# Performance work log

Measured on AMD Instinct MI355X. Metric: run time of the kernel, lower is better.

Reference implementation:

```python
import jax, jax.numpy as jnp
import numpy as np

EPS = 1e-13

def masked_softmax(scores, mask):
    # scores: [B, L1, L2], mask: [B, L2] binary float
    # ESIM-style: softmax(scores * mask) * mask, renormalized.
    m = mask[:, None, :]                      # [B, 1, L2]
    r = jax.nn.softmax(scores * m, axis=-1) * m
    return r / (r.sum(axis=-1, keepdims=True) + EPS)

def weighted_sum(attn, tensor, mask):
    # attn: [B, L1, L2], tensor: [B, L2, D], mask: [B, L1]
    return jnp.matmul(attn, tensor) * mask[:, :, None]

def setup_inputs() -> dict:
    key = jax.random.key(0)
    k1, k2, k3, k4 = jax.random.split(key, 4)
    B, Lp, Lh, D = 64, 512, 512, 600
    encoded_premise = jax.random.normal(k1, (B, Lp, D), dtype=jnp.float32)
    encoded_hypothesis = jax.random.normal(k2, (B, Lh, D), dtype=jnp.float32)
    # binary padding masks (1 = valid token)
    premise_mask = (jax.random.uniform(k3, (B, Lp)) > 0.15).astype(jnp.float32)
    hypothesis_mask = (jax.random.uniform(k4, (B, Lh)) > 0.15).astype(jnp.float32)
    return {"encoded_premise": encoded_premise, "premise_mask": premise_mask,
            "encoded_hypothesis": encoded_hypothesis, "hypothesis_mask": hypothesis_mask}

def reference(encoded_premise, premise_mask, encoded_hypothesis, hypothesis_mask):
    # shared cross-attention score matrix [B, Lp, Lh]
    attn = jnp.einsum('bpd,bhd->bph', encoded_premise, encoded_hypothesis)
    a_p = masked_softmax(attn, hypothesis_mask)                    # [B, Lp, Lh]
    a_h = masked_softmax(attn.transpose(0, 2, 1), premise_mask)    # [B, Lh, Lp]
    weighted_premise = weighted_sum(a_p, encoded_hypothesis, premise_mask)      # [B, Lp, D]
    weighted_hypothesis = weighted_sum(a_h, encoded_premise, hypothesis_mask)   # [B, Lh, D]
    return (weighted_premise, weighted_hypothesis)
```

## Files before the change

### kernel.cpp

```cpp
#include <hip/hip_runtime.h>
#include <hip/hip_bf16.h>

#define DEVB 64
#define LSEQ 512
#define DDIM 600

typedef short short8 __attribute__((ext_vector_type(8)));
typedef float f32x4 __attribute__((ext_vector_type(4)));
typedef _Float16 f16x8 __attribute__((ext_vector_type(8)));
typedef _Float16 f16x4 __attribute__((ext_vector_type(4)));

constexpr int LDP = 40;

__device__ __forceinline__ unsigned short f2bf(float x) {
    union { float f; unsigned u; } v; v.f = x;
    unsigned r = v.u + 0x7fffu + ((v.u >> 16) & 1u);
    return (unsigned short)(r >> 16);
}
__device__ __forceinline__ f32x4 mfma16(short8 a, short8 b, f32x4 c) {
    return __builtin_amdgcn_mfma_f32_16x16x32_bf16(a, b, c, 0, 0, 0);
}
__device__ __forceinline__ f32x4 mfma16h(f16x8 a, f16x8 b, f32x4 c) {
    return __builtin_amdgcn_mfma_f32_16x16x32_f16(a, b, c, 0, 0, 0);
}

__global__ __launch_bounds__(256) void prep_t(
    const float* __restrict__ X, _Float16* __restrict__ Xhi,
    _Float16* __restrict__ Xlo, _Float16* __restrict__ XT)
{
    int blk = blockIdx.x;
    int b   = blk / 80;
    int rem = blk % 80;
    int r0  = (rem / 10) << 6;
    int d0  = (rem % 10) << 6;
    const float* Xb = X + (size_t)b * LSEQ * DDIM;
    _Float16* Hib = Xhi + (size_t)b * LSEQ * DDIM;
    _Float16* Lob = Xlo ? (Xlo + (size_t)b * LSEQ * DDIM) : nullptr;

    __shared__ _Float16 T[64 * 66];
    int t = threadIdx.x;
#pragma unroll
    for (int it = 0; it < 4; ++it) {
        int g  = t + (it << 8);
        int ri = g >> 4;
        int dc = (g & 15) << 2;
        if (d0 + dc < DDIM) {
            float4 x = *(const float4*)(Xb + (size_t)(r0 + ri) * DDIM + d0 + dc);
            f16x4 hi, lo;
            hi[0] = (_Float16)x.x; lo[0] = (_Float16)(x.x - (float)hi[0]);
            hi[1] = (_Float16)x.y; lo[1] = (_Float16)(x.y - (float)hi[1]);
            hi[2] = (_Float16)x.z; lo[2] = (_Float16)(x.z - (float)hi[2]);
            hi[3] = (_Float16)x.w; lo[3] = (_Float16)(x.w - (float)hi[3]);
            *(f16x4*)(Hib + (size_t)(r0 + ri) * DDIM + d0 + dc) = hi;
            if (Lob) *(f16x4*)(Lob + (size_t)(r0 + ri) * DDIM + d0 + dc) = lo;
            T[(dc + 0) * 66 + ri] = hi[0];
            T[(dc + 1) * 66 + ri] = hi[1];
            T[(dc + 2) * 66 + ri] = hi[2];
            T[(dc + 3) * 66 + ri] = hi[3];
        }
    }
    if (XT) {
        __syncthreads();
        int d  = t >> 2;
        int ch = (t & 3) << 4;
        if (d0 + d < DDIM) {
            unsigned buf[8];
#pragma unroll
            for (int i = 0; i < 8; ++i)
                buf[i] = *(const unsigned*)&T[d * 66 + ch + 2 * i];
            unsigned* dst = (unsigned*)(XT + ((size_t)b * DDIM + d0 + d) * LSEQ + r0 + ch);
            *(uint4*)(dst)     = *(uint4*)&buf[0];
            *(uint4*)(dst + 4) = *(uint4*)&buf[4];
        }
    }
}

__global__ __launch_bounds__(256) void attn_gemm(
    const _Float16* __restrict__ Phi, const _Float16* __restrict__ Plo,
    const _Float16* __restrict__ Hhi, float* __restrict__ attn)
{
    const int bid = blockIdx.x;
    const int swz = (bid & 7) * 128 + (bid >> 3);
    const int b  = swz >> 4;
    const int pt = ((swz >> 2) & 3) << 7;
    const int ht = (swz & 3) << 7;
    const _Float16* Pbh = Phi + ((size_t)b * LSEQ + pt) * DDIM;
    const _Float16* Pbl = Plo + ((size_t)b * LSEQ + pt) * DDIM;
    const _Float16* Hb  = Hhi + ((size_t)b * LSEQ + ht) * DDIM;
    float* Ab = attn + (size_t)b * LSEQ * LSEQ;

    __shared__ _Float16 Ah[2][128 * LDP], Al[2][128 * LDP], Bh[2][128 * LDP];

    const int t    = threadIdx.x;
    const int lane = t & 63;
    const int wave = t >> 6;
    const int wm = (wave >> 1) << 6;
    const int wn = (wave & 1) << 6;
    const int fr = lane & 15;
    const int fq = lane >> 4;
    const int srow = t >> 2;
    const int sc8  = (t & 3) << 3;

    f16x8 pf[6];
    const f16x8 zz = {0, 0, 0, 0, 0, 0, 0, 0};
    auto issue = [&](int k0) {
        bool ok = (k0 + sc8) < DDIM;
#pragma unroll
        for (int r = 0; r < 2; ++r) {
            size_t off = (size_t)(srow + (r << 6)) * DDIM + k0 + sc8;
            pf[r * 3 + 0] = ok ? *(const f16x8*)(Pbh + off) : zz;
            pf[r * 3 + 1] = ok ? *(const f16x8*)(Pbl + off) : zz;
            pf[r * 3 + 2] = ok ? *(const f16x8*)(Hb  + off) : zz;
        }
    };
    auto wr = [&](int buf) {
#pragma unroll
        for (int r = 0; r < 2; ++r) {
            int row = srow + (r << 6);
            *(f16x8*)&Ah[buf][row * LDP + sc8] = pf[r * 3 + 0];
            *(f16x8*)&Al[buf][row * LDP + sc8] = pf[r * 3 + 1];
            *(f16x8*)&Bh[buf][row * LDP + sc8] = pf[r * 3 + 2];
        }
    };

    issue(0);
    wr(0);
    issue(32);
    __syncthreads();

    f32x4 acc[4][4];
#pragma unroll
    for (int i = 0; i < 4; ++i)
#pragma unroll
        for (int j = 0; j < 4; ++j) acc[i][j] = (f32x4){0.f, 0.f, 0.f, 0.f};

    constexpr int NK = 19;
    int cur = 0;
    for (int it = 0; it < NK; ++it) {
        f16x8 ah[4], al[4], bh[4];
#pragma unroll
        for (int i = 0; i < 4; ++i) {
            ah[i] = *(const f16x8*)&Ah[cur][(wm + (i << 4) + fr) * LDP + (fq << 3)];
            al[i] = *(const f16x8*)&Al[cur][(wm + (i << 4) + fr) * LDP + (fq << 3)];
            bh[i] = *(const f16x8*)&Bh[cur][(wn + (i << 4) + fr) * LDP + (fq << 3)];
        }
        if (it + 1 < NK) {
            wr(cur ^ 1);
            if (it + 2 < NK) issue((it + 2) << 5);
        }
#pragma unroll
        for (int mi = 0; mi < 4; ++mi)
#pragma unroll
            for (int ni = 0; ni < 4; ++ni) {
                f32x4 c = acc[mi][ni];
                c = mfma16h(ah[mi], bh[ni], c);
                c = mfma16h(al[mi], bh[ni], c);
                acc[mi][ni] = c;
            }
        __syncthreads();
        cur ^= 1;
    }

#pragma unroll
    for (int mi = 0; mi < 4; ++mi)
#pragma unroll
        for (int ni = 0; ni < 4; ++ni)
#pragma unroll
            for (int j = 0; j < 4; ++j) {
                int p = pt + wm + (mi << 4) + (fq << 2) + j;
                int h = ht + wn + (ni << 4) + fr;
                Ab[(size_t)p * LSEQ + h] = acc[mi][ni][j];
            }
}

__global__ __launch_bounds__(256) void stats_w1(
    const float* __restrict__ attn, const float* __restrict__ hmask,
    const float* __restrict__ pmask,
    float* __restrict__ M1, float* __restrict__ R1,
    _Float16* __restrict__ W1,
    float* __restrict__ Mp, float* __restrict__ Tp, float* __restrict__ Sp)
{
    int b      = blockIdx.x >> 3;
    int stripe = blockIdx.x & 7;
    int lane   = threadIdx.x & 63;
    int wave   = threadIdx.x >> 6;
    const float* hm = hmask + (b << 9);
    const float* pm = pmask + (b << 9);

    float4 m0 = *(const float4*)(hm + (lane << 3));
    float4 m1 = *(const float4*)(hm + (lane << 3) + 4);
    float mk[8] = {m0.x, m0.y, m0.z, m0.w, m1.x, m1.y, m1.z, m1.w};

    float cM[8], cT[8], cS[8];
#pragma unroll
    for (int j = 0; j < 8; ++j) { cM[j] = -1e30f; cT[j] = 0.f; cS[j] = 0.f; }

    for (int i = 0; i < 16; ++i) {
        int row   = (stripe << 6) + (wave << 4) + i;
        int rowid = (b << 9) + row;
        const float* rp = attn + (size_t)rowid * LSEQ + (lane << 3);
        float4 s0 = *(const float4*)rp;
        float4 s1 = *(const float4*)(rp + 4);
        float s[8] = {s0.x, s0.y, s0.z, s0.w, s1.x, s1.y, s1.z, s1.w};

        float v[8];
#pragma unroll
        for (int j = 0; j < 8; ++j) v[j] = s[j] * mk[j];
        float mx = -1e30f;
#pragma unroll
        for (int j = 0; j < 8; ++j) mx = fmaxf(mx, v[j]);
#pragma unroll
        for (int off = 32; off; off >>= 1) mx = fmaxf(mx, __shfl_xor(mx, off));

        float e[8], T = 0.f, S = 0.f;
#pragma unroll
        for (int j = 0; j < 8; ++j) { e[j] = __expf(v[j] - mx); T += mk[j] * e[j]; S += e[j]; }
#pragma unroll
        for (int off = 32; off; off >>= 1) { T += __shfl_xor(T, off); S += __shfl_xor(S, off); }
        float R = 1.f / (T + 1e-13f * S);

        if (W1) {
            union { f16x8 v8; _Float16 h[8]; } wv;
#pragma unroll
            for (int j = 0; j < 8; ++j) wv.h[j] = (_Float16)(mk[j] * e[j] * R);
            *(f16x8*)(W1 + (size_t)rowid * LSEQ + (lane << 3)) = wv.v8;
        }
        if (lane == 0) { M1[rowid] = mx; R1[rowid] = R; }

        float pmv = pm[row];
#pragma unroll
        for (int j = 0; j < 8; ++j) {
            float v2 = s[j] * pmv;
            float nm = fmaxf(cM[j], v2);
            float sc = __expf(cM[j] - nm);
            float e2 = __expf(v2 - nm);
            cT[j] = cT[j] * sc + pmv * e2;
            cS[j] = cS[j] * sc + e2;
            cM[j] = nm;
        }
    }

    __shared__ float LM[4][512], LT[4][512], LS[4][512];
#pragma unroll
    for (int j = 0; j < 8; ++j) {
        int c = (lane << 3) + j;
        LM[wave][c] = cM[j]; LT[wave][c] = cT[j]; LS[wave][c] = cS[j];
    }
    __syncthreads();

    size_t base = (size_t)((b << 3) + stripe) * 512;
    for (int cc = threadIdx.x; cc < 512; cc += 256) {
        float gm = fmaxf(fmaxf(LM[0][cc], LM[1][cc]), fmaxf(LM[2][cc], LM[3][cc]));
        float gT = 0.f, gS = 0.f;
#pragma unroll
        for (int w = 0; w < 4; ++w) {
            float sc = __expf(LM[w][cc] - gm);
            gT += LT[w][cc] * sc;
            gS += LS[w][cc] * sc;
        }
        Mp[base + cc] = gm; Tp[base + cc] = gT; Sp[base + cc] = gS;
    }
}

__global__ __launch_bounds__(256) void col_merge(
    const float* __restrict__ Mp, const float* __restrict__ Tp,
    const float* __restrict__ Sp, float* __restrict__ M2, float* __restrict__ R2)
{
    int b = blockIdx.x >> 1;
    int c = ((blockIdx.x & 1) << 8) + threadIdx.x;
    float gm = -1e30f, gT = 0.f, gS = 0.f;
#pragma unroll
    for (int st = 0; st < 8; ++st) {
        size_t idx = (size_t)((b << 3) + st) * 512 + c;
        float m = Mp[idx], tt = Tp[idx], ss = Sp[idx];
        float nm  = fmaxf(gm, m);
        float sc1 = __expf(gm - nm), sc2 = __expf(m - nm);
        gT = gT * sc1 + tt * sc2;
        gS = gS * sc1 + ss * sc2;
        gm = nm;
    }
    M2[(b << 9) + c] = gm;
    R2[(b << 9) + c] = 1.f / (gT + 1e-13f * gS);
}

__global__ __launch_bounds__(256) void w2gen(
    const float* __restrict__ attn, const float* __restrict__ pmask,
    const float* __restrict__ M2, const float* __restrict__ R2,
    _Float16* __restrict__ W2)
{
    int blk = blockIdx.x;
    int b  = blk >> 5;
    int p0 = ((blk >> 2) & 7) << 6;
    int h0 = (blk & 3) << 7;
    const float* Ab = attn + (size_t)b * LSEQ * LSEQ;
    const float* pm = pmask + (b << 9);

    __shared__ float sM[128], sR[128];
    __shared__ _Float16 T[128 * 66];
    int t = threadIdx.x;
    if (t < 128) { sM[t] = M2[(b << 9) + h0 + t]; sR[t] = R2[(b << 9) + h0 + t]; }
    __syncthreads();

#pragma unroll
    for (int it = 0; it < 8; ++it) {
        int g  = t + (it << 8);
        int pi = g >> 5;
        int hc = (g & 31) << 2;
        float4 x = *(const float4*)(Ab + (size_t)(p0 + pi) * LSEQ + h0 + hc);
        float pv = pm[p0 + pi];
        _Float16 w0 = 0, w1 = 0, w2 = 0, w3 = 0;
        if (pv != 0.f) {
            w0 = (_Float16)(__expf(x.x - sM[hc + 0]) * sR[hc + 0]);
            w1 = (_Float16)(__expf(x.y - sM[hc + 1]) * sR[hc + 1]);
            w2 = (_Float16)(__expf(x.z - sM[hc + 2]) * sR[hc + 2]);
            w3 = (_Float16)(__expf(x.w - sM[hc + 3]) * sR[hc + 3]);
        }
        T[(hc + 0) * 66 + pi] = w0;
        T[(hc + 1) * 66 + pi] = w1;
        T[(hc + 2) * 66 + pi] = w2;
        T[(hc + 3) * 66 + pi] = w3;
    }
    __syncthreads();

    int h  = t >> 1;
    int po = (t & 1) << 5;
    unsigned buf[16];
#pragma unroll
    for (int i = 0; i < 16; ++i)
        buf[i] = *(const unsigned*)&T[h * 66 + po + 2 * i];
    unsigned* dst = (unsigned*)(W2 + ((size_t)(b << 9) + h0 + h) * LSEQ + p0 + po);
#pragma unroll
    for (int i = 0; i < 4; ++i)
        *(uint4*)(dst + 4 * i) = *(uint4*)&buf[4 * i];
}

__global__ __launch_bounds__(256) void gemm_fp16(
    const _Float16* __restrict__ W, const _Float16* __restrict__ BT,
    const float* __restrict__ mask_m, float* __restrict__ out)
{
    const int bid = blockIdx.x;
    const int swz = (bid & 7) * 160 + (bid >> 3);
    const int b   = swz / 20;
    const int rem = swz % 20;
    const int m0  = (rem / 5) << 7;
    const int n0  = (rem % 5) << 7;
    const _Float16* Wb = W  + (size_t)b * LSEQ * LSEQ;
    const _Float16* Bb = BT + (size_t)b * DDIM * LSEQ;

    __shared__ _Float16 Wl[2][128 * LDP];
    __shared__ _Float16 Bl[2][128 * LDP];
    __shared__ float Mm[128];

    const int t    = threadIdx.x;
    const int lane = t & 63;
    const int wave = t >> 6;
    const int wm = (wave >> 1) << 6;
    const int wn = (wave & 1) << 6;
    const int fr = lane & 15;
    const int fq = lane >> 4;
    const int srow = t >> 2;
    const int sc8  = (t & 3) << 3;

    if (t < 128) Mm[t] = mask_m[(b << 9) + m0 + t];

    f16x8 pw[2], pb[2];
    const f16x8 zz = {0, 0, 0, 0, 0, 0, 0, 0};
    auto issue = [&](int k0) {
#pragma unroll
        for (int r = 0; r < 2; ++r) {
            int row = srow + (r << 6);
            pw[r] = *(const f16x8*)(Wb + (size_t)(m0 + row) * LSEQ + k0 + sc8);
            int nrow = n0 + row;
            pb[r] = (nrow < DDIM) ? *(const f16x8*)(Bb + (size_t)nrow * LSEQ + k0 + sc8) : zz;
        }
    };
    auto wr = [&](int buf) {
#pragma unroll
        for (int r = 0; r < 2; ++r) {
            int row = srow + (r << 6);
            *(f16x8*)&Wl[buf][row * LDP + sc8] = pw[r];
            *(f16x8*)&Bl[buf][row * LDP + sc8] = pb[r];
        }
    };

    issue(0);
    wr(0);
    issue(32);
    __syncthreads();

    f32x4 acc[4][4];
#pragma unroll
    for (int i = 0; i < 4; ++i)
#pragma unroll
        for (int j = 0; j < 4; ++j) acc[i][j] = (f32x4){0.f, 0.f, 0.f, 0.f};

    constexpr int NK = 16;
    int cur = 0;
    for (int it = 0; it < NK; ++it) {
        f16x8 af[4], bfr[4];
#pragma unroll
        for (int i = 0; i < 4; ++i) {
            af[i]  = *(const f16x8*)&Wl[cur][(wm + (i << 4) + fr) * LDP + (fq << 3)];
            bfr[i] = *(const f16x8*)&Bl[cur][(wn + (i << 4) + fr) * LDP + (fq << 3)];
        }
        if (it + 1 < NK) {
            wr(cur ^ 1);
            if (it + 2 < NK) issue((it + 2) << 5);
        }
#pragma unroll
        for (int mi = 0; mi < 4; ++mi)
#pragma unroll
            for (int ni = 0; ni < 4; ++ni)
                acc[mi][ni] = mfma16h(af[mi], bfr[ni], acc[mi][ni]);
        __syncthreads();
        cur ^= 1;
    }

#pragma unroll
    for (int mi = 0; mi < 4; ++mi)
#pragma unroll
        for (int j = 0; j < 4; ++j) {
            int row = wm + (mi << 4) + (fq << 2) + j;
            float mm = Mm[row];
#pragma unroll
            for (int ni = 0; ni < 4; ++ni) {
                int d = n0 + wn + (ni << 4) + fr;
                if (d < DDIM)
                    out[((size_t)(b << 9) + m0 + row) * DDIM + d] = mm * acc[mi][ni][j];
            }
        }
}

template <int TRANSA>
__global__ __launch_bounds__(256) void wsum(
    const float* __restrict__ attn, const float* __restrict__ Bsrc,
    const float* __restrict__ mask_k, const float* __restrict__ mask_m,
    const float* __restrict__ Mst, const float* __restrict__ Rst,
    float* __restrict__ out)
{
    const int blk = blockIdx.x;
    const int b   = blk / 20;
    const int rem = blk % 20;
    const int m0  = (rem / 5) << 7;
    const int n0  = (rem % 5) << 7;

    const float* Ab  = attn + (size_t)b * LSEQ * LSEQ;
    const float* Bb  = Bsrc + (size_t)b * LSEQ * DDIM;
    const float* mkb = mask_k + (b << 9);

    __shared__ unsigned short Wl[128 * LDP];
    __shared__ unsigned short Bl[128 * LDP];
    __shared__ float Ml[128], Rl[128], Mm[128];

    const int t    = threadIdx.x;
    const int lane = t & 63;
    const int wave = t >> 6;
    const int wm = (wave >> 1) << 6;
    const int wn = (wave & 1) << 6;
    const int fr = lane & 15;
    const int fq = lane >> 4;

    if (t < 128) {
        Ml[t] = Mst[(b << 9) + m0 + t];
        Rl[t] = Rst[(b << 9) + m0 + t];
        Mm[t] = mask_m[(b << 9) + m0 + t];
    }
    __syncthreads();

    f32x4 acc[4][4];
#pragma unroll
    for (int i = 0; i < 4; ++i)
#pragma unroll
        for (int j = 0; j < 4; ++j) acc[i][j] = (f32x4){0.f, 0.f, 0.f, 0.f};

    for (int k0 = 0; k0 < LSEQ; k0 += 32) {
        if constexpr (TRANSA == 0) {
#pragma unroll
            for (int r = 0; r < 4; ++r) {
                int idx = t + (r << 8);
                int row = idx >> 3;
                int c4  = (idx & 7) << 2;
                float4 x  = *(const float4*)(Ab + (size_t)(m0 + row) * LSEQ + k0 + c4);
                float4 km = *(const float4*)(mkb + k0 + c4);
                float Mv = Ml[row], Rv = Rl[row];
                ushort4 w;
                w.x = (km.x != 0.f) ? f2bf(__expf(x.x - Mv) * Rv) : (unsigned short)0;
                w.y = (km.y != 0.f) ? f2bf(__expf(x.y - Mv) * Rv) : (unsigned short)0;
                w.z = (km.z != 0.f) ? f2bf(__expf(x.z - Mv) * Rv) : (unsigned short)0;
                w.w = (km.w != 0.f) ? f2bf(__expf(x.w - Mv) * Rv) : (unsigned short)0;
                *(ushort4*)&Wl[row * LDP + c4] = w;
            }
        } else {
#pragma unroll
            for (int r = 0; r < 4; ++r) {
                int mh = t & 127;
                int pq = (t >> 7) + (r << 1);
                float Mv = Ml[mh], Rv = Rl[mh];
                ushort4 w;
#pragma unroll
                for (int j = 0; j < 4; ++j) {
                    int k = k0 + (pq << 2) + j;
                    float x  = Ab[(size_t)k * LSEQ + m0 + mh];
                    float km = mkb[k];
                    ((unsigned short*)&w)[j] =
                        (km != 0.f) ? f2bf(__expf(x - Mv) * Rv) : (unsigned short)0;
                }
                *(ushort4*)&Wl[mh * LDP + (pq << 2)] = w;
            }
        }
#pragma unroll
        for (int r = 0; r < 4; ++r) {
            int d  = t & 127;
            int kq = (t >> 7) + (r << 1);
            bool valid = (n0 + d) < DDIM;
            ushort4 v;
#pragma unroll
            for (int j = 0; j < 4; ++j) {
                int k = k0 + (kq << 2) + j;
                float x = valid ? Bb[(size_t)k * DDIM + n0 + d] : 0.f;
                ((unsigned short*)&v)[j] = f2bf(x);
            }
            *(ushort4*)&Bl[d * LDP + (kq << 2)] = v;
        }
        __syncthreads();

        short8 af[4], bfr[4];
#pragma unroll
        for (int i = 0; i < 4; ++i) {
            af[i]  = *(const short8*)&Wl[(wm + (i << 4) + fr) * LDP + (fq << 3)];
            bfr[i] = *(const short8*)&Bl[(wn + (i << 4) + fr) * LDP + (fq << 3)];
        }
#pragma unroll
        for (int mi = 0; mi < 4; ++mi)
#pragma unroll
            for (int ni = 0; ni < 4; ++ni)
                acc[mi][ni] = mfma16(af[mi], bfr[ni], acc[mi][ni]);
        __syncthreads();
    }

#pragma unroll
    for (int mi = 0; mi < 4; ++mi)
#pragma unroll
        for (int j = 0; j < 4; ++j) {
            int row = wm + (mi << 4) + (fq << 2) + j;
            float mm = Mm[row];
#pragma unroll
            for (int ni = 0; ni < 4; ++ni) {
                int d = n0 + wn + (ni << 4) + fr;
                if (d < DDIM)
                    out[((size_t)(b << 9) + m0 + row) * DDIM + d] = mm * acc[mi][ni][j];
            }
        }
}

extern "C" void kernel_launch(void* const* d_in, const int* in_sizes, int n_in,
                              void* d_out, int out_size, void* d_ws, size_t ws_size,
                              hipStream_t stream)
{
    const float* P  = (const float*)d_in[0];
    const float* pm = (const float*)d_in[1];
    const float* H  = (const float*)d_in[2];
    const float* hm = (const float*)d_in[3];
    float* out = (float*)d_out;
    char* o  = (char*)d_out;
    char* ws = (char*)d_ws;

    const size_t E = (size_t)DEVB * LSEQ * DDIM;

    _Float16* Phi = (_Float16*)o;
    _Float16* Plo = Phi + E;
    _Float16* Hhi = Plo + E;
    _Float16* hT  = Hhi + E;
    _Float16* W1  = Hhi;

    const size_t fast_need = 143654912;

    if (ws_size >= fast_need) {
        float*     attn = (float*)ws;
        _Float16*  pT   = (_Float16*)(ws + 67108864);
        _Float16*  W2   = (_Float16*)(ws + 67108864 + 39321600);
        float*     Mp   = (float*)(ws + 139984896);
        float*     Tp   = Mp + (size_t)DEVB * 8 * 512;
        float*     Sp   = Tp + (size_t)DEVB * 8 * 512;
        float*     M1   = Sp + (size_t)DEVB * 8 * 512;
        float*     R1   = M1 + DEVB * LSEQ;
        float*     M2   = R1 + DEVB * LSEQ;
        float*     R2   = M2 + DEVB * LSEQ;

        prep_t<<<DEVB * 80, 256, 0, stream>>>(P, Phi, Plo, pT);
        prep_t<<<DEVB * 80, 256, 0, stream>>>(H, Hhi, nullptr, hT);
        attn_gemm<<<DEVB * 16, 256, 0, stream>>>(Phi, Plo, Hhi, attn);
        stats_w1<<<DEVB * 8, 256, 0, stream>>>(attn, hm, pm, M1, R1, W1, Mp, Tp, Sp);
        col_merge<<<DEVB * 2, 256, 0, stream>>>(Mp, Tp, Sp, M2, R2);
        w2gen<<<DEVB * 32, 256, 0, stream>>>(attn, pm, M2, R2, W2);
        gemm_fp16<<<DEVB * 20, 256, 0, stream>>>(W1, hT, pm, out);
        gemm_fp16<<<DEVB * 20, 256, 0, stream>>>(W2, pT, hm, out + E);
    } else {
        float* attn = (float*)ws;
        float* Mp   = (float*)(ws + 67108864);
        float* Tp   = Mp + (size_t)DEVB * 8 * 512;
        float* Sp   = Tp + (size_t)DEVB * 8 * 512;
        float* M1   = Sp + (size_t)DEVB * 8 * 512;
        float* R1   = M1 + DEVB * LSEQ;
        float* M2   = R1 + DEVB * LSEQ;
        float* R2   = M2 + DEVB * LSEQ;

        prep_t<<<DEVB * 80, 256, 0, stream>>>(P, Phi, Plo, nullptr);
        prep_t<<<DEVB * 80, 256, 0, stream>>>(H, Hhi, nullptr, nullptr);
        attn_gemm<<<DEVB * 16, 256, 0, stream>>>(Phi, Plo, Hhi, attn);
        stats_w1<<<DEVB * 8, 256, 0, stream>>>(attn, hm, pm, M1, R1, nullptr, Mp, Tp, Sp);
        col_merge<<<DEVB * 2, 256, 0, stream>>>(Mp, Tp, Sp, M2, R2);
        wsum<0><<<DEVB * 20, 256, 0, stream>>>(attn, H, hm, pm, M1, R1, out);
        wsum<1><<<DEVB * 20, 256, 0, stream>>>(attn, P, pm, hm, M2, R2, out + E);
    }
}
```

Baseline: 327.1 us.

## Merge prep launches, fold column merge into W2 gen, XOR-swizzle LDS tiles

The two input-prep launches become one kernel that picks premise or hypothesis by block index. The column-statistics merge is recomputed inside the W2 generation kernel, so the col_merge launch and its M2/R2 round trip are gone. The GEMM shared-memory tiles drop their padded stride of 40 for an unpadded stride of 32 with an XOR swizzle on 16-byte chunks, which avoids bank conflicts while using less LDS. The cost is redundant merge work per W2 block (each column set is recomputed by 8 blocks) and the mask in the gemm epilogue is now read from global memory instead of shared memory.

```diff
diff --git a/kernel.cpp b/kernel.cpp
--- a/kernel.cpp
+++ b/kernel.cpp
@@ -24,11 +24,17 @@
     return __builtin_amdgcn_mfma_f32_16x16x32_f16(a, b, c, 0, 0, 0);
 }
 
-__global__ __launch_bounds__(256) void prep_t(
-    const float* __restrict__ X, _Float16* __restrict__ Xhi,
-    _Float16* __restrict__ Xlo, _Float16* __restrict__ XT)
+__global__ __launch_bounds__(256) void prep_both(
+    const float* __restrict__ P, const float* __restrict__ H,
+    _Float16* __restrict__ Phi, _Float16* __restrict__ Plo,
+    _Float16* __restrict__ Hhi,
+    _Float16* __restrict__ pT, _Float16* __restrict__ hT)
 {
     int blk = blockIdx.x;
+    const float* X; _Float16 *Xhi, *Xlo, *XT;
+    if (blk < DEVB * 80) { X = P; Xhi = Phi; Xlo = Plo; XT = pT; }
+    else { blk -= DEVB * 80; X = H; Xhi = Hhi; Xlo = nullptr; XT = hT; }
+
     int b   = blk / 80;
     int rem = blk % 80;
     int r0  = (rem / 10) << 6;
@@ -89,7 +95,7 @@
     const _Float16* Hb  = Hhi + ((size_t)b * LSEQ + ht) * DDIM;
     float* Ab = attn + (size_t)b * LSEQ * LSEQ;
 
-    __shared__ _Float16 Ah[2][128 * LDP], Al[2][128 * LDP], Bh[2][128 * LDP];
+    __shared__ _Float16 Ah[2][128 * 32], Al[2][128 * 32], Bh[2][128 * 32];
 
     const int t    = threadIdx.x;
     const int lane = t & 63;
@@ -101,6 +107,10 @@
     const int srow = t >> 2;
     const int sc8  = (t & 3) << 3;
 
+    const int wchunk = (t & 3) ^ (srow & 3);
+    const int woff   = srow * 32 + (wchunk << 3);
+    const int rcoff  = ((fq ^ (fr & 3)) << 3);
+
     f16x8 pf[6];
     const f16x8 zz = {0, 0, 0, 0, 0, 0, 0, 0};
     auto issue = [&](int k0) {
@@ -116,10 +126,10 @@
     auto wr = [&](int buf) {
 #pragma unroll
         for (int r = 0; r < 2; ++r) {
-            int row = srow + (r << 6);
-            *(f16x8*)&Ah[buf][row * LDP + sc8] = pf[r * 3 + 0];
-            *(f16x8*)&Al[buf][row * LDP + sc8] = pf[r * 3 + 1];
-            *(f16x8*)&Bh[buf][row * LDP + sc8] = pf[r * 3 + 2];
+            int off = woff + (r << 11);
+            *(f16x8*)&Ah[buf][off] = pf[r * 3 + 0];
+            *(f16x8*)&Al[buf][off] = pf[r * 3 + 1];
+            *(f16x8*)&Bh[buf][off] = pf[r * 3 + 2];
         }
     };
 
@@ -140,9 +150,11 @@
         f16x8 ah[4], al[4], bh[4];
 #pragma unroll
         for (int i = 0; i < 4; ++i) {
-            ah[i] = *(const f16x8*)&Ah[cur][(wm + (i << 4) + fr) * LDP + (fq << 3)];
-            al[i] = *(const f16x8*)&Al[cur][(wm + (i << 4) + fr) * LDP + (fq << 3)];
-            bh[i] = *(const f16x8*)&Bh[cur][(wn + (i << 4) + fr) * LDP + (fq << 3)];
+            int ra = (wm + (i << 4) + fr) * 32 + rcoff;
+            int rb = (wn + (i << 4) + fr) * 32 + rcoff;
+            ah[i] = *(const f16x8*)&Ah[cur][ra];
+            al[i] = *(const f16x8*)&Al[cur][ra];
+            bh[i] = *(const f16x8*)&Bh[cur][rb];
         }
         if (it + 1 < NK) {
             wr(cur ^ 1);
@@ -283,10 +295,10 @@
     R2[(b << 9) + c] = 1.f / (gT + 1e-13f * gS);
 }
 
-__global__ __launch_bounds__(256) void w2gen(
+__global__ __launch_bounds__(256) void w2gen_m(
     const float* __restrict__ attn, const float* __restrict__ pmask,
-    const float* __restrict__ M2, const float* __restrict__ R2,
-    _Float16* __restrict__ W2)
+    const float* __restrict__ Mp, const float* __restrict__ Tp,
+    const float* __restrict__ Sp, _Float16* __restrict__ W2)
 {
     int blk = blockIdx.x;
     int b  = blk >> 5;
@@ -298,7 +310,21 @@
     __shared__ float sM[128], sR[128];
     __shared__ _Float16 T[128 * 66];
     int t = threadIdx.x;
-    if (t < 128) { sM[t] = M2[(b << 9) + h0 + t]; sR[t] = R2[(b << 9) + h0 + t]; }
+    if (t < 128) {
+        float gm = -1e30f, gT = 0.f, gS = 0.f;
+#pragma unroll
+        for (int st = 0; st < 8; ++st) {
+            size_t idx = (size_t)((b << 3) + st) * 512 + h0 + t;
+            float m = Mp[idx], tt = Tp[idx], ss = Sp[idx];
+            float nm  = fmaxf(gm, m);
+            float sc1 = __expf(gm - nm), sc2 = __expf(m - nm);
+            gT = gT * sc1 + tt * sc2;
+            gS = gS * sc1 + ss * sc2;
+            gm = nm;
+        }
+        sM[t] = gm;
+        sR[t] = 1.f / (gT + 1e-13f * gS);
+    }
     __syncthreads();
 
 #pragma unroll
@@ -347,9 +373,8 @@
     const _Float16* Wb = W  + (size_t)b * LSEQ * LSEQ;
     const _Float16* Bb = BT + (size_t)b * DDIM * LSEQ;
 
-    __shared__ _Float16 Wl[2][128 * LDP];
-    __shared__ _Float16 Bl[2][128 * LDP];
-    __shared__ float Mm[128];
+    __shared__ _Float16 Wl[2][128 * 32];
+    __shared__ _Float16 Bl[2][128 * 32];
 
     const int t    = threadIdx.x;
     const int lane = t & 63;
@@ -361,7 +386,9 @@
     const int srow = t >> 2;
     const int sc8  = (t & 3) << 3;
 
-    if (t < 128) Mm[t] = mask_m[(b << 9) + m0 + t];
+    const int wchunk = (t & 3) ^ (srow & 3);
+    const int woff   = srow * 32 + (wchunk << 3);
+    const int rcoff  = ((fq ^ (fr & 3)) << 3);
 
     f16x8 pw[2], pb[2];
     const f16x8 zz = {0, 0, 0, 0, 0, 0, 0, 0};
@@ -377,9 +404,9 @@
     auto wr = [&](int buf) {
 #pragma unroll
         for (int r = 0; r < 2; ++r) {
-            int row = srow + (r << 6);
-            *(f16x8*)&Wl[buf][row * LDP + sc8] = pw[r];
-            *(f16x8*)&Bl[buf][row * LDP + sc8] = pb[r];
+            int off = woff + (r << 11);
+            *(f16x8*)&Wl[buf][off] = pw[r];
+            *(f16x8*)&Bl[buf][off] = pb[r];
         }
     };
 
@@ -400,8 +427,8 @@
         f16x8 af[4], bfr[4];
 #pragma unroll
         for (int i = 0; i < 4; ++i) {
-            af[i]  = *(const f16x8*)&Wl[cur][(wm + (i << 4) + fr) * LDP + (fq << 3)];
-            bfr[i] = *(const f16x8*)&Bl[cur][(wn + (i << 4) + fr) * LDP + (fq << 3)];
+            af[i]  = *(const f16x8*)&Wl[cur][(wm + (i << 4) + fr) * 32 + rcoff];
+            bfr[i] = *(const f16x8*)&Bl[cur][(wn + (i << 4) + fr) * 32 + rcoff];
         }
         if (it + 1 < NK) {
             wr(cur ^ 1);
@@ -416,12 +443,13 @@
         cur ^= 1;
     }
 
+    const float* mmb = mask_m + (b << 9) + m0;
 #pragma unroll
     for (int mi = 0; mi < 4; ++mi)
 #pragma unroll
         for (int j = 0; j < 4; ++j) {
             int row = wm + (mi << 4) + (fq << 2) + j;
-            float mm = Mm[row];
+            float mm = mmb[row];
 #pragma unroll
             for (int ni = 0; ni < 4; ++ni) {
                 int d = n0 + wn + (ni << 4) + fr;
@@ -584,15 +612,11 @@
         float*     Sp   = Tp + (size_t)DEVB * 8 * 512;
         float*     M1   = Sp + (size_t)DEVB * 8 * 512;
         float*     R1   = M1 + DEVB * LSEQ;
-        float*     M2   = R1 + DEVB * LSEQ;
-        float*     R2   = M2 + DEVB * LSEQ;
-
-        prep_t<<<DEVB * 80, 256, 0, stream>>>(P, Phi, Plo, pT);
-        prep_t<<<DEVB * 80, 256, 0, stream>>>(H, Hhi, nullptr, hT);
+
+        prep_both<<<DEVB * 160, 256, 0, stream>>>(P, H, Phi, Plo, Hhi, pT, hT);
         attn_gemm<<<DEVB * 16, 256, 0, stream>>>(Phi, Plo, Hhi, attn);
         stats_w1<<<DEVB * 8, 256, 0, stream>>>(attn, hm, pm, M1, R1, W1, Mp, Tp, Sp);
-        col_merge<<<DEVB * 2, 256, 0, stream>>>(Mp, Tp, Sp, M2, R2);
-        w2gen<<<DEVB * 32, 256, 0, stream>>>(attn, pm, M2, R2, W2);
+        w2gen_m<<<DEVB * 32, 256, 0, stream>>>(attn, pm, Mp, Tp, Sp, W2);
         gemm_fp16<<<DEVB * 20, 256, 0, stream>>>(W1, hT, pm, out);
         gemm_fp16<<<DEVB * 20, 256, 0, stream>>>(W2, pT, hm, out + E);
     } else {
@@ -605,8 +629,7 @@
         float* M2   = R1 + DEVB * LSEQ;
         float* R2   = M2 + DEVB * LSEQ;
 
-        prep_t<<<DEVB * 80, 256, 0, stream>>>(P, Phi, Plo, nullptr);
-        prep_t<<<DEVB * 80, 256, 0, stream>>>(H, Hhi, nullptr, nullptr);
+        prep_both<<<DEVB * 160, 256, 0, stream>>>(P, H, Phi, Plo, Hhi, nullptr, nullptr);
         attn_gemm<<<DEVB * 16, 256, 0, stream>>>(Phi, Plo, Hhi, attn);
         stats_w1<<<DEVB * 8, 256, 0, stream>>>(attn, hm, pm, M1, R1, nullptr, Mp, Tp, Sp);
         col_merge<<<DEVB * 2, 256, 0, stream>>>(Mp, Tp, Sp, M2, R2);
```

After: 345.1 us. 1.06x slower.
